# Performance work log

Measured on AMD Instinct MI355X. Metric: run time of the kernel, lower is better.

## Reference

```python
import jax, jax.numpy as jnp
import numpy as np

N = 8192
D_IN, D_MID, D_EMB = 1024, 256, 64
N_EDGES = N * 8


def setup_inputs() -> dict:
    key = jax.random.key(0)
    ks = jax.random.split(key, 6)
    X = jax.random.normal(ks[0], (N, D_IN), dtype=jnp.float32)
    # Xavier-uniform style init as in get_weight_initial
    b1 = np.sqrt(6.0 / (D_IN + D_MID))
    b2 = np.sqrt(6.0 / (D_MID + D_EMB))
    W1 = jax.random.uniform(ks[1], (D_IN, D_MID), minval=-b1, maxval=b1, dtype=jnp.float32)
    W2 = jax.random.uniform(ks[2], (D_MID, D_EMB), minval=-b2, maxval=b2, dtype=jnp.float32)
    edge_val = jax.random.uniform(ks[3], (N_EDGES,), dtype=jnp.float32)
    edge_src = jax.random.randint(ks[4], (N_EDGES,), 0, N, dtype=jnp.int32)
    edge_dst = jax.random.randint(ks[5], (N_EDGES,), 0, N, dtype=jnp.int32)
    return {"X": X, "W1": W1, "W2": W2, "edge_val": edge_val,
            "edge_src": edge_src, "edge_dst": edge_dst}


def reference(X, W1, W2, edge_val, edge_src, edge_dst):
    n = X.shape[0]

    def spmm(H):  # sparse Laplacian (COO) times dense H
        return jax.ops.segment_sum(edge_val[:, None] * H[edge_src], edge_dst,
                                   num_segments=n)

    h = jax.nn.relu(spmm(X @ W1))          # [N, D_MID]
    emb = spmm(h @ W2)                      # [N, D_EMB]
    # pairwise squared Euclidean distances between rows of emb -> [N, N]
    sq = jnp.sum(emb * emb, axis=1)
    dist = sq[:, None] + sq[None, :] - 2.0 * (emb @ emb.T)
    recons_w = jax.nn.softmax(-dist, axis=1) + 1e-10
    return recons_w
```

## Files before the change

### kernel.cpp

```cpp
#include <hip/hip_runtime.h>
#include <cstddef>

constexpr int NN    = 8192;
constexpr int DIN   = 1024;
constexpr int DMID  = 256;
constexpr int DEMB  = 64;
constexpr int NEDGE = 65536;

typedef __attribute__((ext_vector_type(8))) short bf16x8;
typedef __attribute__((ext_vector_type(4))) float f32x4;
#define MFMA16(a, b, c) __builtin_amdgcn_mfma_f32_16x16x32_bf16((a), (b), (c), 0, 0, 0)

__device__ __forceinline__ unsigned short bf16_rne(float x) {
  unsigned u = __float_as_uint(x);
  return (unsigned short)((u + 0x7FFFu + ((u >> 16) & 1u)) >> 16);
}
__device__ __forceinline__ float bf16_tof(unsigned short h) {
  return __uint_as_float((unsigned)h << 16);
}

constexpr int WCONV_BLOCKS = (DMID * DIN + DEMB * DMID) / 256;
__global__ __launch_bounds__(256) void prep_kernel(const float* __restrict__ W1,
                                                   const float* __restrict__ W2,
                                                   unsigned short* __restrict__ W1b,
                                                   unsigned short* __restrict__ W2b,
                                                   const int* __restrict__ edst,
                                                   int* __restrict__ counts)
{
  int b = blockIdx.x;
  if (b < WCONV_BLOCKS) {
    int idx = b * 256 + threadIdx.x;
    if (idx < DMID * DIN) {
      int n = idx >> 10, k = idx & 1023;
      W1b[idx] = bf16_rne(W1[k * DMID + n]);
    } else {
      int t = idx - DMID * DIN;
      int n = t >> 8, k = t & 255;
      W2b[t] = bf16_rne(W2[k * DEMB + n]);
    }
  } else {
    int e = (b - WCONV_BLOCKS) * 256 + threadIdx.x;
    atomicAdd(&counts[edst[e]], 1);
  }
}

__global__ __launch_bounds__(256) void scan_kernel(const int* __restrict__ counts,
                                                   int* __restrict__ row_start)
{
  __shared__ int sums[256];
  const int t = threadIdx.x;
  int local[32];
  int s = 0;
#pragma unroll
  for (int i = 0; i < 32; ++i) { local[i] = counts[t * 32 + i]; s += local[i]; }
  sums[t] = s;
  __syncthreads();
  for (int off = 1; off < 256; off <<= 1) {
    int v = (t >= off) ? sums[t - off] : 0;
    __syncthreads();
    sums[t] += v;
    __syncthreads();
  }
  int base = (t == 0) ? 0 : sums[t - 1];
#pragma unroll
  for (int i = 0; i < 32; ++i) { row_start[t * 32 + i] = base; base += local[i]; }
  if (t == 255) row_start[NN] = base;
}

__global__ __launch_bounds__(256) void scatter_kernel(
    const int* __restrict__ src, const float* __restrict__ val,
    const int* __restrict__ dst, const int* __restrict__ row_start,
    int* __restrict__ cursor, int* __restrict__ csr_src, float* __restrict__ csr_val)
{
  int e = blockIdx.x * 256 + threadIdx.x;
  int d = dst[e];
  int pos = row_start[d] + atomicAdd(&cursor[d], 1);
  csr_src[pos] = src[e];
  csr_val[pos] = val[e];
}

__global__ __launch_bounds__(256) void gemm1_kernel(
    const float* __restrict__ X, const unsigned short* __restrict__ W1b,
    unsigned short* __restrict__ G1)
{
  const int lane = threadIdx.x & 63;
  const int wave = threadIdx.x >> 6;
  const int m0 = blockIdx.y * 64 + wave * 16;
  const int n0 = blockIdx.x * 64;
  const int rl = lane & 15;
  const int kq = (lane >> 4) * 8;
  f32x4 zero = {0.f, 0.f, 0.f, 0.f};
  f32x4 acc[4] = {zero, zero, zero, zero};
  for (int s = 0; s < DIN / 32; ++s) {
    const int kb = s * 32 + kq;
    const float* xp = X + (size_t)(m0 + rl) * DIN + kb;
    float4 x0 = *(const float4*)xp;
    float4 x1 = *(const float4*)(xp + 4);
    bf16x8 ah;
    ah[0] = (short)bf16_rne(x0.x); ah[1] = (short)bf16_rne(x0.y);
    ah[2] = (short)bf16_rne(x0.z); ah[3] = (short)bf16_rne(x0.w);
    ah[4] = (short)bf16_rne(x1.x); ah[5] = (short)bf16_rne(x1.y);
    ah[6] = (short)bf16_rne(x1.z); ah[7] = (short)bf16_rne(x1.w);
#pragma unroll
    for (int ns = 0; ns < 4; ++ns) {
      bf16x8 bh = *(const bf16x8*)(W1b + (size_t)(n0 + ns * 16 + rl) * DIN + kb);
      acc[ns] = MFMA16(ah, bh, acc[ns]);
    }
  }
  const int rq = (lane >> 4) * 4;
#pragma unroll
  for (int ns = 0; ns < 4; ++ns)
#pragma unroll
    for (int r = 0; r < 4; ++r)
      G1[(size_t)(m0 + rq + r) * DMID + n0 + ns * 16 + rl] = bf16_rne(acc[ns][r]);
}

__global__ __launch_bounds__(256) void spmm1_kernel(
    const unsigned short* __restrict__ G1, const int* __restrict__ row_start,
    const int* __restrict__ csr_src, const float* __restrict__ csr_val,
    unsigned short* __restrict__ Hb)
{
  const int lane = threadIdx.x & 63;
  const int wave = threadIdx.x >> 6;
  const int r = blockIdx.x * 4 + wave;
  const int e0 = row_start[r];
  const int e1 = row_start[r + 1];
  const int c = lane * 4;
  float4 acc = make_float4(0.f, 0.f, 0.f, 0.f);
  for (int e = e0; e < e1; ++e) {
    const int s   = csr_src[e];
    const float v = csr_val[e];
    ushort4 h = *(const ushort4*)(G1 + (size_t)s * DMID + c);
    acc.x = fmaf(v, bf16_tof(h.x), acc.x);
    acc.y = fmaf(v, bf16_tof(h.y), acc.y);
    acc.z = fmaf(v, bf16_tof(h.z), acc.z);
    acc.w = fmaf(v, bf16_tof(h.w), acc.w);
  }
  ushort4 h;
  h.x = bf16_rne(fmaxf(acc.x, 0.f));
  h.y = bf16_rne(fmaxf(acc.y, 0.f));
  h.z = bf16_rne(fmaxf(acc.z, 0.f));
  h.w = bf16_rne(fmaxf(acc.w, 0.f));
  *(ushort4*)(Hb + (size_t)r * DMID + c) = h;
}

__global__ __launch_bounds__(256) void gemm2_kernel(
    const unsigned short* __restrict__ Ab, const unsigned short* __restrict__ W2b,
    float* __restrict__ E1)
{
  const int lane = threadIdx.x & 63;
  const int wave = threadIdx.x >> 6;
  const int m0 = blockIdx.x * 64 + wave * 16;
  const int rl = lane & 15;
  const int kq = (lane >> 4) * 8;
  f32x4 zero = {0.f, 0.f, 0.f, 0.f};
  f32x4 acc[4] = {zero, zero, zero, zero};
  for (int s = 0; s < DMID / 32; ++s) {
    const int kb = s * 32 + kq;
    bf16x8 ah = *(const bf16x8*)(Ab + (size_t)(m0 + rl) * DMID + kb);
#pragma unroll
    for (int ns = 0; ns < 4; ++ns) {
      bf16x8 bh = *(const bf16x8*)(W2b + (size_t)(ns * 16 + rl) * DMID + kb);
      acc[ns] = MFMA16(ah, bh, acc[ns]);
    }
  }
  const int rq = (lane >> 4) * 4;
#pragma unroll
  for (int ns = 0; ns < 4; ++ns)
#pragma unroll
    for (int r = 0; r < 4; ++r)
      E1[(size_t)(m0 + rq + r) * DEMB + ns * 16 + rl] = acc[ns][r];
}

__global__ __launch_bounds__(256) void spmm2_kernel(
    const float* __restrict__ H, const int* __restrict__ row_start,
    const int* __restrict__ csr_src, const float* __restrict__ csr_val,
    unsigned short* __restrict__ EmbH, float* __restrict__ sqv)
{
  const int lane = threadIdx.x & 63;
  const int wave = threadIdx.x >> 6;
  const int r = blockIdx.x * 4 + wave;
  const int e0 = row_start[r];
  const int e1 = row_start[r + 1];
  float acc = 0.f;
  for (int e = e0; e < e1; ++e)
    acc = fmaf(csr_val[e], H[(size_t)csr_src[e] * DEMB + lane], acc);
  unsigned short h = bf16_rne(acc);
  EmbH[(size_t)r * DEMB + lane] = h;
  float hf = bf16_tof(h);
  float sq = hf * hf;
#pragma unroll
  for (int off = 32; off; off >>= 1) sq += __shfl_xor(sq, off, 64);
  if (lane == 0) sqv[r] = sq;
}

__device__ __forceinline__ void dist_tile_hh(
    const unsigned short* __restrict__ EH, int ibase, int jbase, int lane,
    f32x4 (&acc)[4][4])
{
  const int rl = lane & 15;
  const int kq = (lane >> 4) * 8;
#pragma unroll
  for (int s = 0; s < 2; ++s) {
    const int kb = s * 32 + kq;
    bf16x8 a[4], b[4];
#pragma unroll
    for (int t = 0; t < 4; ++t) {
      a[t] = *(const bf16x8*)(EH + (size_t)(ibase + t * 16 + rl) * DEMB + kb);
      b[t] = *(const bf16x8*)(EH + (size_t)(jbase + t * 16 + rl) * DEMB + kb);
    }
#pragma unroll
    for (int ms = 0; ms < 4; ++ms)
#pragma unroll
      for (int ns = 0; ns < 4; ++ns)
        acc[ms][ns] = MFMA16(a[ms], b[ns], acc[ms][ns]);
  }
}

__global__ __launch_bounds__(256) void rowsum_sym_kernel(
    const unsigned short* __restrict__ EH, const float* __restrict__ sq,
    float* __restrict__ rowsum)
{
  const int bi = blockIdx.y, bj = blockIdx.x;
  if (bj < bi) return;
  const int lane = threadIdx.x & 63;
  const int wave = threadIdx.x >> 6;
  const int wr = wave >> 1, wc = wave & 1;
  const int ibase = bi * 128 + wr * 64;
  const int jbase = bj * 128 + wc * 64;
  const int rl = lane & 15;
  const int rq = (lane >> 4) * 4;

  f32x4 zero = {0.f, 0.f, 0.f, 0.f};
  f32x4 acc[4][4];
#pragma unroll
  for (int ms = 0; ms < 4; ++ms)
#pragma unroll
    for (int ns = 0; ns < 4; ++ns) acc[ms][ns] = zero;
  dist_tile_hh(EH, ibase, jbase, lane, acc);

  float si[4][4], sj[4];
#pragma unroll
  for (int ms = 0; ms < 4; ++ms)
#pragma unroll
    for (int r = 0; r < 4; ++r) si[ms][r] = sq[ibase + ms * 16 + rq + r];
#pragma unroll
  for (int ns = 0; ns < 4; ++ns) sj[ns] = sq[jbase + ns * 16 + rl];

  float rs[4][4] = {};
  float cs[4]    = {};
#pragma unroll
  for (int ms = 0; ms < 4; ++ms)
#pragma unroll
    for (int ns = 0; ns < 4; ++ns)
#pragma unroll
      for (int r = 0; r < 4; ++r) {
        float v = __expf(fmaf(2.f, acc[ms][ns][r], -si[ms][r] - sj[ns]));
        rs[ms][r] += v;
        cs[ns]    += v;
      }

#pragma unroll
  for (int ms = 0; ms < 4; ++ms)
#pragma unroll
    for (int r = 0; r < 4; ++r) {
      float v = rs[ms][r];
      v += __shfl_xor(v, 1, 64);
      v += __shfl_xor(v, 2, 64);
      v += __shfl_xor(v, 4, 64);
      v += __shfl_xor(v, 8, 64);
      if (rl == 0) atomicAdd(&rowsum[ibase + ms * 16 + rq + r], v);
    }

  if (bi != bj) {
#pragma unroll
    for (int ns = 0; ns < 4; ++ns) {
      float v = cs[ns];
      v += __shfl_xor(v, 16, 64);
      v += __shfl_xor(v, 32, 64);
      if (lane < 16) atomicAdd(&rowsum[jbase + ns * 16 + rl], v);
    }
  }
}

__global__ __launch_bounds__(256) void dist_write_kernel(
    const unsigned short* __restrict__ EH, const float* __restrict__ sq,
    const float* __restrict__ rowsum, float* __restrict__ out)
{
  const int lane = threadIdx.x & 63;
  const int wave = threadIdx.x >> 6;
  const int wr = wave >> 1, wc = wave & 1;
  const int ibase = blockIdx.y * 128 + wr * 64;
  const int jbase = blockIdx.x * 128 + wc * 64;
  const int rl = lane & 15;
  const int rq = (lane >> 4) * 4;

  f32x4 zero = {0.f, 0.f, 0.f, 0.f};
  f32x4 acc[4][4];
#pragma unroll
  for (int ms = 0; ms < 4; ++ms)
#pragma unroll
    for (int ns = 0; ns < 4; ++ns) acc[ms][ns] = zero;
  dist_tile_hh(EH, ibase, jbase, lane, acc);

  float si[4][4], ri[4][4], sj[4];
#pragma unroll
  for (int ms = 0; ms < 4; ++ms)
#pragma unroll
    for (int r = 0; r < 4; ++r) {
      const int i = ibase + ms * 16 + rq + r;
      si[ms][r] = sq[i];
      ri[ms][r] = 1.f / rowsum[i];
    }
#pragma unroll
  for (int ns = 0; ns < 4; ++ns) sj[ns] = sq[jbase + ns * 16 + rl];

#pragma unroll
  for (int ms = 0; ms < 4; ++ms)
#pragma unroll
    for (int r = 0; r < 4; ++r) {
      const size_t row = (size_t)(ibase + ms * 16 + rq + r) * NN;
#pragma unroll
      for (int ns = 0; ns < 4; ++ns) {
        float e = __expf(fmaf(2.f, acc[ms][ns][r], -si[ms][r] - sj[ns]));
        out[row + jbase + ns * 16 + rl] = fmaf(e, ri[ms][r], 1e-10f);
      }
    }
}

extern "C" void kernel_launch(void* const* d_in, const int* in_sizes, int n_in,
                              void* d_out, int out_size, void* d_ws, size_t ws_size,
                              hipStream_t stream)
{
  const float* X  = (const float*)d_in[0];
  const float* W1 = (const float*)d_in[1];
  const float* W2 = (const float*)d_in[2];
  const float* ev = (const float*)d_in[3];
  const int* esrc = (const int*)d_in[4];
  const int* edst = (const int*)d_in[5];
  float* out = (float*)d_out;

  char* p = (char*)d_ws;
  auto alloc = [&](size_t bytes) { char* q = p; p += (bytes + 255) & ~(size_t)255; return q; };

  int*   counts    = (int*)alloc(NN * 4);
  int*   cursor    = (int*)alloc(NN * 4);
  float* rowsum    = (float*)alloc(NN * 4);
  int*   row_start = (int*)alloc((NN + 1) * 4);
  int*   csr_src   = (int*)alloc(NEDGE * 4);
  float* csr_val   = (float*)alloc(NEDGE * 4);
  float* sqv       = (float*)alloc(NN * 4);
  float* E1        = (float*)alloc((size_t)NN * DEMB * 4);
  unsigned short* W1b  = (unsigned short*)alloc((size_t)DMID * DIN * 2);
  unsigned short* W2b  = (unsigned short*)alloc((size_t)DEMB * DMID * 2);
  unsigned short* G1   = (unsigned short*)alloc((size_t)NN * DMID * 2);
  unsigned short* H1b  = (unsigned short*)alloc((size_t)NN * DMID * 2);
  unsigned short* EmbH = (unsigned short*)alloc((size_t)NN * DEMB * 2);

  hipMemsetAsync(d_ws, 0, (size_t)3 * NN * 4, stream);

  prep_kernel<<<WCONV_BLOCKS + NEDGE / 256, 256, 0, stream>>>(W1, W2, W1b, W2b, edst, counts);
  scan_kernel<<<1, 256, 0, stream>>>(counts, row_start);
  scatter_kernel<<<NEDGE / 256, 256, 0, stream>>>(esrc, ev, edst, row_start, cursor,
                                                  csr_src, csr_val);

  gemm1_kernel<<<dim3(DMID / 64, NN / 64), 256, 0, stream>>>(X, W1b, G1);
  spmm1_kernel<<<NN / 4, 256, 0, stream>>>(G1, row_start, csr_src, csr_val, H1b);
  gemm2_kernel<<<NN / 64, 256, 0, stream>>>(H1b, W2b, E1);
  spmm2_kernel<<<NN / 4, 256, 0, stream>>>(E1, row_start, csr_src, csr_val, EmbH, sqv);

  rowsum_sym_kernel<<<dim3(NN / 128, NN / 128), 256, 0, stream>>>(EmbH, sqv, rowsum);
  dist_write_kernel<<<dim3(NN / 128, NN / 128), 256, 0, stream>>>(EmbH, sqv, rowsum, out);
}
```

Baseline: 459.2 us.

## Fuse CSR build into one cooperative kernel and widen gemm1 N-tile

Replaces the memset plus the separate prep, scan and scatter kernels with a single cooperative kernel that uses grid-wide syncs. This removes several launches and their gaps. Separately, gemm1 now computes 128 output columns per block instead of 64, so each converted X fragment is reused across twice as many MFMAs and X is re-read half as often. The risks are the overhead of grid.sync and higher register pressure in gemm1, which also halves the grid size.

```diff
diff --git a/kernel.cpp b/kernel.cpp
--- a/kernel.cpp
+++ b/kernel.cpp
@@ -1,5 +1,8 @@
 #include <hip/hip_runtime.h>
+#include <hip/hip_cooperative_groups.h>
 #include <cstddef>
+
+namespace cg = cooperative_groups;
 
 constexpr int NN    = 8192;
 constexpr int DIN   = 1024;
@@ -19,17 +22,20 @@
   return __uint_as_float((unsigned)h << 16);
 }
 
-constexpr int WCONV_BLOCKS = (DMID * DIN + DEMB * DMID) / 256;
-__global__ __launch_bounds__(256) void prep_kernel(const float* __restrict__ W1,
-                                                   const float* __restrict__ W2,
-                                                   unsigned short* __restrict__ W1b,
-                                                   unsigned short* __restrict__ W2b,
-                                                   const int* __restrict__ edst,
-                                                   int* __restrict__ counts)
-{
-  int b = blockIdx.x;
-  if (b < WCONV_BLOCKS) {
-    int idx = b * 256 + threadIdx.x;
+__global__ __launch_bounds__(256) void build_kernel(
+    const float* __restrict__ W1, const float* __restrict__ W2,
+    unsigned short* __restrict__ W1b, unsigned short* __restrict__ W2b,
+    const int* __restrict__ edst, const int* __restrict__ esrc,
+    const float* __restrict__ ev,
+    int* __restrict__ counts, int* __restrict__ cursor, float* __restrict__ rowsum,
+    int* __restrict__ row_start, int* __restrict__ csr_src, float* __restrict__ csr_val)
+{
+  cg::grid_group grid = cg::this_grid();
+  const int tid = blockIdx.x * 256 + threadIdx.x;
+
+  if (tid < 3 * NN) counts[tid] = 0;
+  constexpr int WTOT = DMID * DIN + DEMB * DMID;
+  for (int idx = tid; idx < WTOT; idx += 65536) {
     if (idx < DMID * DIN) {
       int n = idx >> 10, k = idx & 1023;
       W1b[idx] = bf16_rne(W1[k * DMID + n]);
@@ -38,45 +44,40 @@
       int n = t >> 8, k = t & 255;
       W2b[t] = bf16_rne(W2[k * DEMB + n]);
     }
-  } else {
-    int e = (b - WCONV_BLOCKS) * 256 + threadIdx.x;
-    atomicAdd(&counts[edst[e]], 1);
-  }
-}
-
-__global__ __launch_bounds__(256) void scan_kernel(const int* __restrict__ counts,
-                                                   int* __restrict__ row_start)
-{
-  __shared__ int sums[256];
-  const int t = threadIdx.x;
-  int local[32];
-  int s = 0;
-#pragma unroll
-  for (int i = 0; i < 32; ++i) { local[i] = counts[t * 32 + i]; s += local[i]; }
-  sums[t] = s;
-  __syncthreads();
-  for (int off = 1; off < 256; off <<= 1) {
-    int v = (t >= off) ? sums[t - off] : 0;
+  }
+  grid.sync();
+
+  atomicAdd(&counts[edst[tid]], 1);
+  grid.sync();
+
+  if (blockIdx.x == 0) {
+    __shared__ int sums[256];
+    const int t = threadIdx.x;
+    int local[32];
+    int s = 0;
+#pragma unroll
+    for (int i = 0; i < 32; ++i) { local[i] = counts[t * 32 + i]; s += local[i]; }
+    sums[t] = s;
     __syncthreads();
-    sums[t] += v;
-    __syncthreads();
-  }
-  int base = (t == 0) ? 0 : sums[t - 1];
-#pragma unroll
-  for (int i = 0; i < 32; ++i) { row_start[t * 32 + i] = base; base += local[i]; }
-  if (t == 255) row_start[NN] = base;
-}
-
-__global__ __launch_bounds__(256) void scatter_kernel(
-    const int* __restrict__ src, const float* __restrict__ val,
-    const int* __restrict__ dst, const int* __restrict__ row_start,
-    int* __restrict__ cursor, int* __restrict__ csr_src, float* __restrict__ csr_val)
-{
-  int e = blockIdx.x * 256 + threadIdx.x;
-  int d = dst[e];
-  int pos = row_start[d] + atomicAdd(&cursor[d], 1);
-  csr_src[pos] = src[e];
-  csr_val[pos] = val[e];
+    for (int off = 1; off < 256; off <<= 1) {
+      int v = (t >= off) ? sums[t - off] : 0;
+      __syncthreads();
+      sums[t] += v;
+      __syncthreads();
+    }
+    int base = (t == 0) ? 0 : sums[t - 1];
+#pragma unroll
+    for (int i = 0; i < 32; ++i) { row_start[t * 32 + i] = base; base += local[i]; }
+    if (t == 255) row_start[NN] = base;
+  }
+  grid.sync();
+
+  {
+    int d = edst[tid];
+    int pos = row_start[d] + atomicAdd(&cursor[d], 1);
+    csr_src[pos] = esrc[tid];
+    csr_val[pos] = ev[tid];
+  }
 }
 
 __global__ __launch_bounds__(256) void gemm1_kernel(
@@ -86,11 +87,13 @@
   const int lane = threadIdx.x & 63;
   const int wave = threadIdx.x >> 6;
   const int m0 = blockIdx.y * 64 + wave * 16;
-  const int n0 = blockIdx.x * 64;
+  const int n0 = blockIdx.x * 128;
   const int rl = lane & 15;
   const int kq = (lane >> 4) * 8;
   f32x4 zero = {0.f, 0.f, 0.f, 0.f};
-  f32x4 acc[4] = {zero, zero, zero, zero};
+  f32x4 acc[8];
+#pragma unroll
+  for (int ns = 0; ns < 8; ++ns) acc[ns] = zero;
   for (int s = 0; s < DIN / 32; ++s) {
     const int kb = s * 32 + kq;
     const float* xp = X + (size_t)(m0 + rl) * DIN + kb;
@@ -102,14 +105,14 @@
     ah[4] = (short)bf16_rne(x1.x); ah[5] = (short)bf16_rne(x1.y);
     ah[6] = (short)bf16_rne(x1.z); ah[7] = (short)bf16_rne(x1.w);
 #pragma unroll
-    for (int ns = 0; ns < 4; ++ns) {
+    for (int ns = 0; ns < 8; ++ns) {
       bf16x8 bh = *(const bf16x8*)(W1b + (size_t)(n0 + ns * 16 + rl) * DIN + kb);
       acc[ns] = MFMA16(ah, bh, acc[ns]);
     }
   }
   const int rq = (lane >> 4) * 4;
 #pragma unroll
-  for (int ns = 0; ns < 4; ++ns)
+  for (int ns = 0; ns < 8; ++ns)
 #pragma unroll
     for (int r = 0; r < 4; ++r)
       G1[(size_t)(m0 + rq + r) * DMID + n0 + ns * 16 + rl] = bf16_rne(acc[ns][r]);
@@ -357,14 +360,16 @@
   unsigned short* H1b  = (unsigned short*)alloc((size_t)NN * DMID * 2);
   unsigned short* EmbH = (unsigned short*)alloc((size_t)NN * DEMB * 2);
 
-  hipMemsetAsync(d_ws, 0, (size_t)3 * NN * 4, stream);
-
-  prep_kernel<<<WCONV_BLOCKS + NEDGE / 256, 256, 0, stream>>>(W1, W2, W1b, W2b, edst, counts);
-  scan_kernel<<<1, 256, 0, stream>>>(counts, row_start);
-  scatter_kernel<<<NEDGE / 256, 256, 0, stream>>>(esrc, ev, edst, row_start, cursor,
-                                                  csr_src, csr_val);
-
-  gemm1_kernel<<<dim3(DMID / 64, NN / 64), 256, 0, stream>>>(X, W1b, G1);
+  {
+    void* args[] = {(void*)&W1, (void*)&W2, (void*)&W1b, (void*)&W2b,
+                    (void*)&edst, (void*)&esrc, (void*)&ev,
+                    (void*)&counts, (void*)&cursor, (void*)&rowsum,
+                    (void*)&row_start, (void*)&csr_src, (void*)&csr_val};
+    hipLaunchCooperativeKernel((const void*)build_kernel, dim3(256), dim3(256),
+                               args, 0, stream);
+  }
+
+  gemm1_kernel<<<dim3(DMID / 128, NN / 64), 256, 0, stream>>>(X, W1b, G1);
   spmm1_kernel<<<NN / 4, 256, 0, stream>>>(G1, row_start, csr_src, csr_val, H1b);
   gemm2_kernel<<<NN / 64, 256, 0, stream>>>(H1b, W2b, E1);
   spmm2_kernel<<<NN / 4, 256, 0, stream>>>(E1, row_start, csr_src, csr_val, EmbH, sqv);
```

After: 528.6 us. 1.15x slower.
